# Kernel optimization log

Measured on AMD Instinct MI355X. Metric: run time of the kernel, lower is better.

## Reference

```python
import jax, jax.numpy as jnp
import numpy as np

N = 1048576
B = 1024
D = 128


def setup_inputs() -> dict:
    key = jax.random.key(0)
    k1, k2, k3, k4 = jax.random.split(key, 4)
    feat = jax.random.normal(k1, (N, D), dtype=jnp.float32)
    W_gate = jax.random.normal(k2, (D, 1), dtype=jnp.float32) * (1.0 / np.sqrt(D))
    b_gate = jnp.zeros((1,), dtype=jnp.float32)
    W_feat = jax.random.normal(k3, (D, D), dtype=jnp.float32) * (1.0 / np.sqrt(D))
    b_feat = jnp.zeros((D,), dtype=jnp.float32)
    segment_ids = jnp.sort(jax.random.randint(k4, (N,), 0, B)).astype(jnp.int32)
    return {
        "feat": feat,
        "W_gate": W_gate,
        "b_gate": b_gate,
        "W_feat": W_feat,
        "b_feat": b_feat,
        "segment_ids": segment_ids,
        "num_segments": B,
    }


def reference(feat, W_gate, b_gate, W_feat, b_feat, segment_ids, num_segments):
    # gate_nn: Dense(D -> 1); feat_nn: Dense(D -> D)
    gate = feat @ W_gate + b_gate            # [N, 1]
    h = feat @ W_feat + b_feat               # [N, D]
    # segment-wise (per-graph) numerically stable softmax over nodes
    seg_max = jax.ops.segment_max(gate, segment_ids, num_segments=num_segments)  # [B, 1]
    e = jnp.exp(gate - seg_max[segment_ids])                                     # [N, 1]
    denom = jax.ops.segment_sum(e, segment_ids, num_segments=num_segments)       # [B, 1]
    alpha = e / denom[segment_ids]                                               # [N, 1]
    # segment-weighted sum readout -> [B, D]
    return jax.ops.segment_sum(h * alpha, segment_ids, num_segments=num_segments)
```

## Files before the change

kernel.cpp:

```cpp
#include <hip/hip_runtime.h>
#include <math.h>

#define DD 128

__global__ __launch_bounds__(256) void seg_bounds_kernel(
    const int* __restrict__ seg_ids, int* __restrict__ seg_ptr, int n, int nseg)
{
    int b = blockIdx.x * blockDim.x + threadIdx.x;
    if (b > nseg) return;
    if (b == nseg) { seg_ptr[b] = n; return; }
    int lo = 0, hi = n;
    while (lo < hi) {
        int mid = (lo + hi) >> 1;
        if (seg_ids[mid] < b) lo = mid + 1; else hi = mid;
    }
    seg_ptr[b] = lo;
}

__global__ __launch_bounds__(512, 8) void seg_pool_kernel(
    const float* __restrict__ feat,
    const float* __restrict__ W_gate,
    const float* __restrict__ W_feat,
    const float* __restrict__ b_feat,
    const int* __restrict__ seg_ptr,
    float* __restrict__ out)
{
    const int b     = blockIdx.x;
    const int start = seg_ptr[b];
    const int end   = seg_ptr[b + 1];
    const int tid   = threadIdx.x;
    const int lane  = tid & 63;
    const int wave  = tid >> 6;
    const int half  = lane >> 5;
    const int col   = lane & 31;

    if (start >= end) {
        if (tid < DD) out[(size_t)b * DD + tid] = 0.0f;
        return;
    }

    const float4 wg = ((const float4*)W_gate)[col];

    float  l   = 0.0f;
    float4 acc = make_float4(0.0f, 0.0f, 0.0f, 0.0f);

    int r = start + wave * 2 + half;

    const float4 fzero = make_float4(0.0f, 0.0f, 0.0f, 0.0f);
    float4 f0 = (r      < end) ? ((const float4*)(feat + (size_t)(r     ) * DD))[col] : fzero;
    float4 f1 = (r + 16 < end) ? ((const float4*)(feat + (size_t)(r + 16) * DD))[col] : fzero;
    float4 f2 = (r + 32 < end) ? ((const float4*)(feat + (size_t)(r + 32) * DD))[col] : fzero;

    int i = start + wave * 2;
    while (i < end) {
        float4 fn = (r + 48 < end) ? ((const float4*)(feat + (size_t)(r + 48) * DD))[col] : fzero;

        float g = f0.x * wg.x + f0.y * wg.y + f0.z * wg.z + f0.w * wg.w;
        #pragma unroll
        for (int off = 1; off <= 16; off <<= 1)
            g += __shfl_xor(g, off, 64);

        const float e = (r < end) ? __expf(g) : 0.0f;
        l     += e;
        acc.x += e * f0.x;
        acc.y += e * f0.y;
        acc.z += e * f0.z;
        acc.w += e * f0.w;

        f0 = f1; f1 = f2; f2 = fn;
        r += 16; i += 16;
    }

    acc.x += __shfl_xor(acc.x, 32, 64);
    acc.y += __shfl_xor(acc.y, 32, 64);
    acc.z += __shfl_xor(acc.z, 32, 64);
    acc.w += __shfl_xor(acc.w, 32, 64);
    l     += __shfl_xor(l,     32, 64);

    __shared__ float4 s_acc[8][32];
    __shared__ float  s_l[8];
    __shared__ float  s_fbar[DD];

    if (lane < 32) s_acc[wave][col] = acc;
    if (lane == 0) s_l[wave] = l;
    __syncthreads();

    if (wave == 0 && lane < 32) {
        float  L = 0.0f;
        float4 A = make_float4(0.0f, 0.0f, 0.0f, 0.0f);
        #pragma unroll
        for (int w = 0; w < 8; ++w) {
            const float4 a = s_acc[w][col];
            L   += s_l[w];
            A.x += a.x; A.y += a.y; A.z += a.z; A.w += a.w;
        }
        const float inv = 1.0f / L;
        ((float4*)s_fbar)[col] = make_float4(A.x * inv, A.y * inv, A.z * inv, A.w * inv);
    }
    __syncthreads();

    if (tid < DD) {
        float sum = b_feat[tid];
        #pragma unroll 8
        for (int k = 0; k < DD; ++k)
            sum = fmaf(s_fbar[k], W_feat[k * DD + tid], sum);
        out[(size_t)b * DD + tid] = sum;
    }
}

extern "C" void kernel_launch(void* const* d_in, const int* in_sizes, int n_in,
                              void* d_out, int out_size, void* d_ws, size_t ws_size,
                              hipStream_t stream)
{
    const float* feat   = (const float*)d_in[0];
    const float* W_gate = (const float*)d_in[1];
    const float* W_feat = (const float*)d_in[3];
    const float* b_feat = (const float*)d_in[4];
    const int*   segids = (const int*)d_in[5];

    const int n    = in_sizes[5];
    const int nseg = out_size / DD;

    int* seg_ptr = (int*)d_ws;

    seg_bounds_kernel<<<dim3((nseg + 1 + 255) / 256), dim3(256), 0, stream>>>(
        segids, seg_ptr, n, nseg);

    seg_pool_kernel<<<dim3(nseg), dim3(512), 0, stream>>>(
        feat, W_gate, W_feat, b_feat, seg_ptr, (float*)d_out);
}
```

Before: 705.4 us.

## Remap rows to 16-lane groups with DPP reductions and split epilogue GEMV

Each row is now handled by 16 lanes that each load two float4 chunks, so a wave processes four rows per step instead of two. The gate dot product is reduced with DPP adds instead of ds_swizzle shuffles. Loads use clamped row indices in place of predicated branches, and row validity is checked only when the exp weight is applied. The final 128x128 GEMV is split across all 512 threads in four k-groups combined in shared memory, and launch bounds drop to 4 blocks per SM. The intent is less shuffle overhead and more memory-level parallelism. In exchange the kernel uses more registers per thread and more shared memory.

```diff
diff --git a/kernel.cpp b/kernel.cpp
--- a/kernel.cpp
+++ b/kernel.cpp
@@ -2,6 +2,8 @@
 #include <math.h>
 
 #define DD 128
+
+typedef float vf4 __attribute__((ext_vector_type(4)));
 
 __global__ __launch_bounds__(256) void seg_bounds_kernel(
     const int* __restrict__ seg_ids, int* __restrict__ seg_ptr, int n, int nseg)
@@ -17,13 +19,21 @@
     seg_ptr[b] = lo;
 }
 
-__global__ __launch_bounds__(512, 8) void seg_pool_kernel(
+template <int CTRL>
+__device__ __forceinline__ float dpp_add(float x)
+{
+    int t = __builtin_amdgcn_update_dpp(0, __float_as_int(x), CTRL, 0xF, 0xF, true);
+    return x + __int_as_float(t);
+}
+
+__global__ __launch_bounds__(512, 4) void seg_pool_kernel(
     const float* __restrict__ feat,
     const float* __restrict__ W_gate,
     const float* __restrict__ W_feat,
     const float* __restrict__ b_feat,
     const int* __restrict__ seg_ptr,
-    float* __restrict__ out)
+    float* __restrict__ out,
+    int n)
 {
     const int b     = blockIdx.x;
     const int start = seg_ptr[b];
@@ -31,81 +41,114 @@
     const int tid   = threadIdx.x;
     const int lane  = tid & 63;
     const int wave  = tid >> 6;
-    const int half  = lane >> 5;
-    const int col   = lane & 31;
+    const int rgrp  = lane >> 4;
+    const int c     = lane & 15;
 
     if (start >= end) {
         if (tid < DD) out[(size_t)b * DD + tid] = 0.0f;
         return;
     }
 
-    const float4 wg = ((const float4*)W_gate)[col];
+    const vf4 wga = *(const vf4*)(W_gate + c * 4);
+    const vf4 wgb = *(const vf4*)(W_gate + 64 + c * 4);
 
-    float  l   = 0.0f;
-    float4 acc = make_float4(0.0f, 0.0f, 0.0f, 0.0f);
+    const char* fb   = (const char*)feat;
+    const int   nm1  = n - 1;
+    const unsigned colb = (unsigned)c * 16u;
 
-    int r = start + wave * 2 + half;
+    int rp = start + wave * 4 + rgrp;
+    int rc = rp;
 
-    const float4 fzero = make_float4(0.0f, 0.0f, 0.0f, 0.0f);
-    float4 f0 = (r      < end) ? ((const float4*)(feat + (size_t)(r     ) * DD))[col] : fzero;
-    float4 f1 = (r + 16 < end) ? ((const float4*)(feat + (size_t)(r + 16) * DD))[col] : fzero;
-    float4 f2 = (r + 32 < end) ? ((const float4*)(feat + (size_t)(r + 32) * DD))[col] : fzero;
+    unsigned o0 = ((unsigned)min(rp, nm1) << 9) + colb; rp += 32;
+    unsigned o1 = ((unsigned)min(rp, nm1) << 9) + colb; rp += 32;
+    unsigned o2 = ((unsigned)min(rp, nm1) << 9) + colb; rp += 32;
+    vf4 a0 = *(const vf4*)(fb + o0);
+    vf4 b0 = *(const vf4*)(fb + o0 + 256);
+    vf4 a1 = *(const vf4*)(fb + o1);
+    vf4 b1 = *(const vf4*)(fb + o1 + 256);
+    vf4 a2 = *(const vf4*)(fb + o2);
+    vf4 b2 = *(const vf4*)(fb + o2 + 256);
 
-    int i = start + wave * 2;
-    while (i < end) {
-        float4 fn = (r + 48 < end) ? ((const float4*)(feat + (size_t)(r + 48) * DD))[col] : fzero;
+    float l  = 0.0f;
+    vf4   Aa = {0.0f, 0.0f, 0.0f, 0.0f};
+    vf4   Ab = {0.0f, 0.0f, 0.0f, 0.0f};
 
-        float g = f0.x * wg.x + f0.y * wg.y + f0.z * wg.z + f0.w * wg.w;
-        #pragma unroll
-        for (int off = 1; off <= 16; off <<= 1)
-            g += __shfl_xor(g, off, 64);
+    for (int i = start + wave * 4; i < end; i += 32) {
+        unsigned on = ((unsigned)min(rp, nm1) << 9) + colb; rp += 32;
+        vf4 na = *(const vf4*)(fb + on);
+        vf4 nb = *(const vf4*)(fb + on + 256);
 
-        const float e = (r < end) ? __expf(g) : 0.0f;
-        l     += e;
-        acc.x += e * f0.x;
-        acc.y += e * f0.y;
-        acc.z += e * f0.z;
-        acc.w += e * f0.w;
+        float g =      a0.x * wga.x;
+        g = fmaf(a0.y, wga.y, g);
+        g = fmaf(a0.z, wga.z, g);
+        g = fmaf(a0.w, wga.w, g);
+        g = fmaf(b0.x, wgb.x, g);
+        g = fmaf(b0.y, wgb.y, g);
+        g = fmaf(b0.z, wgb.z, g);
+        g = fmaf(b0.w, wgb.w, g);
 
-        f0 = f1; f1 = f2; f2 = fn;
-        r += 16; i += 16;
+        g = dpp_add<0xB1>(g);
+        g = dpp_add<0x4E>(g);
+        g = dpp_add<0x141>(g);
+        g = dpp_add<0x140>(g);
+
+        const float e = (rc < end) ? __expf(g) : 0.0f;
+        rc += 32;
+        l  += e;
+        Aa += e * a0;
+        Ab += e * b0;
+
+        a0 = a1; b0 = b1; a1 = a2; b1 = b2; a2 = na; b2 = nb;
     }
 
-    acc.x += __shfl_xor(acc.x, 32, 64);
-    acc.y += __shfl_xor(acc.y, 32, 64);
-    acc.z += __shfl_xor(acc.z, 32, 64);
-    acc.w += __shfl_xor(acc.w, 32, 64);
-    l     += __shfl_xor(l,     32, 64);
+    l += __shfl_xor(l, 16);
+    l += __shfl_xor(l, 32);
+    #pragma unroll
+    for (int j = 0; j < 4; ++j) {
+        Aa[j] += __shfl_xor(Aa[j], 16);
+        Aa[j] += __shfl_xor(Aa[j], 32);
+        Ab[j] += __shfl_xor(Ab[j], 16);
+        Ab[j] += __shfl_xor(Ab[j], 32);
+    }
 
-    __shared__ float4 s_acc[8][32];
-    __shared__ float  s_l[8];
-    __shared__ float  s_fbar[DD];
+    __shared__ float s_acc[8][DD];
+    __shared__ float s_l[8];
+    __shared__ float s_fbar[DD];
+    __shared__ float s_part[4][DD];
 
-    if (lane < 32) s_acc[wave][col] = acc;
-    if (lane == 0) s_l[wave] = l;
-    __syncthreads();
-
-    if (wave == 0 && lane < 32) {
-        float  L = 0.0f;
-        float4 A = make_float4(0.0f, 0.0f, 0.0f, 0.0f);
+    if (lane < 16) {
         #pragma unroll
-        for (int w = 0; w < 8; ++w) {
-            const float4 a = s_acc[w][col];
-            L   += s_l[w];
-            A.x += a.x; A.y += a.y; A.z += a.z; A.w += a.w;
+        for (int j = 0; j < 4; ++j) {
+            s_acc[wave][c * 4 + j]      = Aa[j];
+            s_acc[wave][64 + c * 4 + j] = Ab[j];
         }
-        const float inv = 1.0f / L;
-        ((float4*)s_fbar)[col] = make_float4(A.x * inv, A.y * inv, A.z * inv, A.w * inv);
+        if (lane == 0) s_l[wave] = l;
     }
     __syncthreads();
 
     if (tid < DD) {
-        float sum = b_feat[tid];
+        float A = 0.0f, L = 0.0f;
+        #pragma unroll
+        for (int w = 0; w < 8; ++w) { A += s_acc[w][tid]; L += s_l[w]; }
+        s_fbar[tid] = A / L;
+    }
+    __syncthreads();
+
+    {
+        const int d  = tid & (DD - 1);
+        const int kg = tid >> 7;
+        float sum = 0.0f;
         #pragma unroll 8
-        for (int k = 0; k < DD; ++k)
-            sum = fmaf(s_fbar[k], W_feat[k * DD + tid], sum);
-        out[(size_t)b * DD + tid] = sum;
+        for (int k = kg * 32; k < kg * 32 + 32; ++k)
+            sum = fmaf(s_fbar[k], W_feat[k * DD + d], sum);
+        s_part[kg][d] = sum;
     }
+    __syncthreads();
+
+    if (tid < DD)
+        out[(size_t)b * DD + tid] =
+            b_feat[tid] + ((s_part[0][tid] + s_part[1][tid]) +
+                           (s_part[2][tid] + s_part[3][tid]));
 }
 
 extern "C" void kernel_launch(void* const* d_in, const int* in_sizes, int n_in,
@@ -127,5 +170,5 @@
         segids, seg_ptr, n, nseg);
 
     seg_pool_kernel<<<dim3(nseg), dim3(512), 0, stream>>>(
-        feat, W_gate, W_feat, b_feat, seg_ptr, (float*)d_out);
+        feat, W_gate, W_feat, b_feat, seg_ptr, (float*)d_out, n);
 }
```

Measured after the change: 698.6 us. No clear change (-1.0%).
